# Kernel optimization log

Hardware: AMD Instinct MI355X
Metric: run time of the kernel (lower is better)

## Reference

```python
import jax, jax.numpy as jnp
import numpy as np

B, M, D, P, T = 512, 16, 128, 16, 4096
GAMMA = 1.0  # similarity_size


def setup_inputs() -> dict:
    key = jax.random.key(0)
    k1, k2, k3, k4, k5 = jax.random.split(key, 5)
    phi = jax.random.normal(k1, (B, P), dtype=jnp.float32)
    state = jax.random.normal(k2, (B, D), dtype=jnp.float32)
    trajectories = jax.random.normal(k3, (T, D), dtype=jnp.float32)
    # Stand-in per-model KAARMA state-transition parameters (linear recurrent + input map, tanh)
    A = jax.random.normal(k4, (M, D, D), dtype=jnp.float32) * (1.0 / np.sqrt(D))
    B_in = jax.random.normal(k5, (M, P, D), dtype=jnp.float32) * (1.0 / np.sqrt(P))
    return {"phi": phi, "state": state, "trajectories": trajectories, "A": A, "B_in": B_in}


def reference(phi, state, trajectories, A, B_in):
    # per-model state update: new_state[b,m,:] = tanh(state @ A_m + phi @ B_m)
    new_state = jnp.tanh(
        jnp.einsum("bd,mdh->bmh", state, A) + jnp.einsum("bp,mph->bmh", phi, B_in)
    )  # [B, M, D]
    # RBF similarity vs trajectory set via ||s||^2 + ||t||^2 - 2 s.t (single batched GEMM)
    s_sq = jnp.sum(new_state * new_state, axis=-1, keepdims=True)      # [B, M, 1]
    t_sq = jnp.sum(trajectories * trajectories, axis=-1)               # [T]
    cross = jnp.einsum("bmd,td->bmt", new_state, trajectories)         # [B, M, T]
    sq_dist = jnp.maximum(s_sq + t_sq[None, None, :] - 2.0 * cross, 0.0)
    sim = jnp.exp(-GAMMA * sq_dist)                                    # [B, M, T]
    output = sim.reshape(phi.shape[0], -1)                             # [B, M*T]
    return output, new_state
```

## Files before the change

kernel.cpp:

```cpp
#include <hip/hip_runtime.h>
#include <hip/hip_bf16.h>
#include <cstdint>
#include <cstddef>

#define NB 512
#define NM 16
#define ND 128
#define NP 16
#define NT 4096

typedef __bf16 bf16x8 __attribute__((ext_vector_type(8)));
typedef float f32x4 __attribute__((ext_vector_type(4)));

static_assert(sizeof(bf16x8) == 16, "bf16x8 must be 16B");

__device__ __forceinline__ void gload_lds16(const void* g, void* l) {
  __builtin_amdgcn_global_load_lds(
      (const __attribute__((address_space(1))) unsigned int*)g,
      (__attribute__((address_space(3))) unsigned int*)l, 16, 0, 0);
}

__global__ __launch_bounds__(256) void prep_kernel(
    const float* __restrict__ phi, const float* __restrict__ state,
    const float* __restrict__ traj, const float* __restrict__ A,
    const float* __restrict__ Bin, float* __restrict__ ns_out,
    __bf16* __restrict__ ns_bf, __bf16* __restrict__ tj_bf,
    float* __restrict__ s_sq, float* __restrict__ t_sq) {
  __shared__ alignas(16) float sSt[16 * 128];
  __shared__ alignas(16) float sPhi[16 * 16];
  __shared__ alignas(16) float sRes[16 * 128];
  const int tid = threadIdx.x;
  const int bx = blockIdx.x;

  if (bx < 512) {
    const int m = bx & 15;
    const int b0 = (bx >> 4) * 16;
    const float4* S4 = (const float4*)(state + (size_t)b0 * 128);
    float4* sSt4 = (float4*)sSt;
    sSt4[tid] = S4[tid];
    sSt4[tid + 256] = S4[tid + 256];
    sPhi[tid] = phi[b0 * 16 + tid];
    __syncthreads();

    const int h2 = tid & 63;
    const int rgrp = tid >> 6;
    const float* Ap = A + (size_t)m * 16384 + h2;
    const float* Bp = Bin + (size_t)m * 2048 + h2;

    float acc[2][4];
#pragma unroll
    for (int hi = 0; hi < 2; ++hi)
#pragma unroll
      for (int j = 0; j < 4; ++j) acc[hi][j] = 0.f;

#pragma unroll 4
    for (int c = 0; c < 32; ++c) {
      float a0[4], a1[4];
#pragma unroll
      for (int u = 0; u < 4; ++u) {
        a0[u] = Ap[(size_t)(c * 4 + u) * 128];
        a1[u] = Ap[(size_t)(c * 4 + u) * 128 + 64];
      }
#pragma unroll
      for (int j = 0; j < 4; ++j) {
        const f32x4 sv = *(const f32x4*)&sSt[(rgrp * 4 + j) * 128 + c * 4];
#pragma unroll
        for (int u = 0; u < 4; ++u) {
          acc[0][j] = fmaf(sv[u], a0[u], acc[0][j]);
          acc[1][j] = fmaf(sv[u], a1[u], acc[1][j]);
        }
      }
    }
#pragma unroll
    for (int pc = 0; pc < 4; ++pc) {
      float b0v[4], b1v[4];
#pragma unroll
      for (int u = 0; u < 4; ++u) {
        b0v[u] = Bp[(size_t)(pc * 4 + u) * 128];
        b1v[u] = Bp[(size_t)(pc * 4 + u) * 128 + 64];
      }
#pragma unroll
      for (int j = 0; j < 4; ++j) {
        const f32x4 pv = *(const f32x4*)&sPhi[(rgrp * 4 + j) * 16 + pc * 4];
#pragma unroll
        for (int u = 0; u < 4; ++u) {
          acc[0][j] = fmaf(pv[u], b0v[u], acc[0][j]);
          acc[1][j] = fmaf(pv[u], b1v[u], acc[1][j]);
        }
      }
    }

#pragma unroll
    for (int j = 0; j < 4; ++j) {
      const int row = rgrp * 4 + j;
      const int R = (b0 + row) * 16 + m;
      const float v0 = tanhf(acc[0][j]);
      const float v1 = tanhf(acc[1][j]);
      ns_out[(size_t)R * 128 + h2] = v0;
      ns_out[(size_t)R * 128 + h2 + 64] = v1;
      sRes[row * 128 + h2] = v0;
      sRes[row * 128 + h2 + 64] = v1;
      float s = v0 * v0 + v1 * v1;
#pragma unroll
      for (int o = 32; o > 0; o >>= 1) s += __shfl_xor(s, o);
      if (h2 == 0) s_sq[R] = s;
    }
    __syncthreads();

    {
      const int row = tid >> 4;
      const int kb = tid & 15;
      const f32x4 r0 = *(const f32x4*)&sRes[row * 128 + kb * 8];
      const f32x4 r1 = *(const f32x4*)&sRes[row * 128 + kb * 8 + 4];
      bf16x8 o;
#pragma unroll
      for (int i = 0; i < 4; ++i) {
        o[i] = (__bf16)r0[i];
        o[i + 4] = (__bf16)r1[i];
      }
      const int R = (b0 + row) * 16 + m;
      *(bf16x8*)(ns_bf + (size_t)R * 128 + ((kb ^ m) * 8)) = o;
    }
  } else {
    const int t0 = (bx - 512) * 128;
    const int t = t0 + (tid >> 1);
    const int half = tid & 1;
    float s = 0.f;
#pragma unroll
    for (int q = 0; q < 8; ++q) {
      const int kb = half * 8 + q;
      const f32x4 v0 = *(const f32x4*)&traj[(size_t)t * 128 + kb * 8];
      const f32x4 v1 = *(const f32x4*)&traj[(size_t)t * 128 + kb * 8 + 4];
      s += v0[0] * v0[0] + v0[1] * v0[1] + v0[2] * v0[2] + v0[3] * v0[3];
      s += v1[0] * v1[0] + v1[1] * v1[1] + v1[2] * v1[2] + v1[3] * v1[3];
      bf16x8 o;
#pragma unroll
      for (int i = 0; i < 4; ++i) {
        o[i] = (__bf16)v0[i];
        o[i + 4] = (__bf16)v1[i];
      }
      *(bf16x8*)(tj_bf + (size_t)t * 128 + ((kb ^ (t & 15)) * 8)) = o;
    }
    s += __shfl_xor(s, 1);
    if (half == 0) t_sq[t] = s;
  }
}

__global__ __launch_bounds__(256) void sim_kernel(
    const __bf16* __restrict__ ns_bf, const __bf16* __restrict__ tj_bf,
    const float* __restrict__ s_sq, const float* __restrict__ t_sq,
    float* __restrict__ out) {
  __shared__ alignas(16) __bf16 sA[128 * 128];
  __shared__ alignas(16) __bf16 sB[128 * 128];
  __shared__ float sSq[128];
  __shared__ float sTq[128];
  const int tid = threadIdx.x;
  const int lane = tid & 63;
  const int w = tid >> 6;
  const int R0 = blockIdx.x * 128;
  const int C0 = blockIdx.y * 128;

  const char* gA = (const char*)(ns_bf + (size_t)R0 * 128);
  const char* gB = (const char*)(tj_bf + (size_t)C0 * 128);
#pragma unroll
  for (int it = 0; it < 8; ++it) {
    const int off = it * 4096 + w * 1024;
    gload_lds16(gA + off + lane * 16, (char*)sA + off);
    gload_lds16(gB + off + lane * 16, (char*)sB + off);
  }
  if (tid < 128)
    sSq[tid] = s_sq[R0 + tid];
  else
    sTq[tid - 128] = t_sq[C0 + tid - 128];
  __syncthreads();

  const int rbase = (w >> 1) * 64;
  const int cbase = (w & 1) * 64;
  const int l15 = lane & 15;
  const int quad = lane >> 4;

  f32x4 acc[4][4];
#pragma unroll
  for (int i = 0; i < 4; ++i)
#pragma unroll
    for (int j = 0; j < 4; ++j) acc[i][j] = (f32x4){0.f, 0.f, 0.f, 0.f};

#pragma unroll
  for (int ks = 0; ks < 4; ++ks) {
    const int kb = quad + ks * 4;
    const int koff = (kb ^ l15) * 8;
    bf16x8 af[4], bfr[4];
#pragma unroll
    for (int i = 0; i < 4; ++i)
      af[i] = *(const bf16x8*)&sA[(rbase + i * 16 + l15) * 128 + koff];
#pragma unroll
    for (int i = 0; i < 4; ++i)
      bfr[i] = *(const bf16x8*)&sB[(cbase + i * 16 + l15) * 128 + koff];
#pragma unroll
    for (int ri = 0; ri < 4; ++ri)
#pragma unroll
      for (int ci = 0; ci < 4; ++ci)
        acc[ri][ci] = __builtin_amdgcn_mfma_f32_16x16x32_bf16(
            bfr[ci], af[ri], acc[ri][ci], 0, 0, 0);
  }

#pragma unroll
  for (int ri = 0; ri < 4; ++ri) {
    const int nsrow = rbase + ri * 16 + l15;
    const float sq = sSq[nsrow];
    float* orow = out + (size_t)(R0 + nsrow) * NT + C0;
#pragma unroll
    for (int ci = 0; ci < 4; ++ci) {
      const int t4 = cbase + ci * 16 + quad * 4;
      const f32x4 tq = *(const f32x4*)&sTq[t4];
      f32x4 r;
#pragma unroll
      for (int k = 0; k < 4; ++k) {
        const float d = fmaxf(sq + tq[k] - 2.f * acc[ri][ci][k], 0.f);
        r[k] = __expf(-d);
      }
      *(f32x4*)&orow[t4] = r;
    }
  }
}

extern "C" void kernel_launch(void* const* d_in, const int* in_sizes, int n_in,
                              void* d_out, int out_size, void* d_ws,
                              size_t ws_size, hipStream_t stream) {
  (void)in_sizes; (void)n_in; (void)out_size; (void)ws_size;
  const float* phi   = (const float*)d_in[0];
  const float* state = (const float*)d_in[1];
  const float* traj  = (const float*)d_in[2];
  const float* A     = (const float*)d_in[3];
  const float* Bin   = (const float*)d_in[4];

  float* out = (float*)d_out;
  float* out_ns = out + (size_t)NB * NM * NT;

  char* ws = (char*)d_ws;
  __bf16* ns_bf = (__bf16*)ws;
  __bf16* tj_bf = (__bf16*)(ws + (2u << 20));
  float* s_sq   = (float*)(ws + (3u << 20));
  float* t_sq   = (float*)(ws + (3u << 20) + (32u << 10));

  prep_kernel<<<544, 256, 0, stream>>>(phi, state, traj, A, Bin, out_ns, ns_bf,
                                       tj_bf, s_sq, t_sq);
  dim3 g2(NB * NM / 128, NT / 128);
  sim_kernel<<<g2, 256, 0, stream>>>(ns_bf, tj_bf, s_sq, t_sq, out);
}
```

Before: 168.7 us.

## Halve sim-kernel A tile in LDS, process rows in two halves, nontemporal stores

The sim kernel now keeps only 64 rows of the state tile in LDS and handles the 128-row block in two halves. The second half is loaded while the first half's epilogue runs. This cuts LDS use (48KB instead of 64KB) and accumulator registers, so more blocks can be resident per CU and output stores can overlap with loads. All output and new_state stores become nontemporal so they do not pollute the cache. The cost is extra barriers and a serialized second GEMM phase per block.

```diff
diff --git a/kernel.cpp b/kernel.cpp
--- a/kernel.cpp
+++ b/kernel.cpp
@@ -96,8 +96,8 @@
       const int R = (b0 + row) * 16 + m;
       const float v0 = tanhf(acc[0][j]);
       const float v1 = tanhf(acc[1][j]);
-      ns_out[(size_t)R * 128 + h2] = v0;
-      ns_out[(size_t)R * 128 + h2 + 64] = v1;
+      __builtin_nontemporal_store(v0, &ns_out[(size_t)R * 128 + h2]);
+      __builtin_nontemporal_store(v1, &ns_out[(size_t)R * 128 + h2 + 64]);
       sRes[row * 128 + h2] = v0;
       sRes[row * 128 + h2 + 64] = v1;
       float s = v0 * v0 + v1 * v1;
@@ -150,8 +150,8 @@
     const __bf16* __restrict__ ns_bf, const __bf16* __restrict__ tj_bf,
     const float* __restrict__ s_sq, const float* __restrict__ t_sq,
     float* __restrict__ out) {
-  __shared__ alignas(16) __bf16 sA[128 * 128];
   __shared__ alignas(16) __bf16 sB[128 * 128];
+  __shared__ alignas(16) __bf16 sA[64 * 128];
   __shared__ float sSq[128];
   __shared__ float sTq[128];
   const int tid = threadIdx.x;
@@ -160,13 +160,17 @@
   const int R0 = blockIdx.x * 128;
   const int C0 = blockIdx.y * 128;
 
+  const char* gB = (const char*)(tj_bf + (size_t)C0 * 128);
   const char* gA = (const char*)(ns_bf + (size_t)R0 * 128);
-  const char* gB = (const char*)(tj_bf + (size_t)C0 * 128);
 #pragma unroll
   for (int it = 0; it < 8; ++it) {
-    const int off = it * 4096 + w * 1024;
+    const int off = w * 8192 + it * 1024;
+    gload_lds16(gB + off + lane * 16, (char*)sB + off);
+  }
+#pragma unroll
+  for (int it = 0; it < 4; ++it) {
+    const int off = w * 4096 + it * 1024;
     gload_lds16(gA + off + lane * 16, (char*)sA + off);
-    gload_lds16(gB + off + lane * 16, (char*)sB + off);
   }
   if (tid < 128)
     sSq[tid] = s_sq[R0 + tid];
@@ -174,53 +178,68 @@
     sTq[tid - 128] = t_sq[C0 + tid - 128];
   __syncthreads();
 
-  const int rbase = (w >> 1) * 64;
+  const int abase = (w >> 1) * 32;
   const int cbase = (w & 1) * 64;
   const int l15 = lane & 15;
   const int quad = lane >> 4;
 
-  f32x4 acc[4][4];
-#pragma unroll
-  for (int i = 0; i < 4; ++i)
-#pragma unroll
-    for (int j = 0; j < 4; ++j) acc[i][j] = (f32x4){0.f, 0.f, 0.f, 0.f};
-
-#pragma unroll
-  for (int ks = 0; ks < 4; ++ks) {
-    const int kb = quad + ks * 4;
-    const int koff = (kb ^ l15) * 8;
-    bf16x8 af[4], bfr[4];
-#pragma unroll
-    for (int i = 0; i < 4; ++i)
-      af[i] = *(const bf16x8*)&sA[(rbase + i * 16 + l15) * 128 + koff];
-#pragma unroll
-    for (int i = 0; i < 4; ++i)
-      bfr[i] = *(const bf16x8*)&sB[(cbase + i * 16 + l15) * 128 + koff];
-#pragma unroll
-    for (int ri = 0; ri < 4; ++ri)
-#pragma unroll
-      for (int ci = 0; ci < 4; ++ci)
-        acc[ri][ci] = __builtin_amdgcn_mfma_f32_16x16x32_bf16(
-            bfr[ci], af[ri], acc[ri][ci], 0, 0, 0);
-  }
-
-#pragma unroll
-  for (int ri = 0; ri < 4; ++ri) {
-    const int nsrow = rbase + ri * 16 + l15;
-    const float sq = sSq[nsrow];
-    float* orow = out + (size_t)(R0 + nsrow) * NT + C0;
-#pragma unroll
-    for (int ci = 0; ci < 4; ++ci) {
-      const int t4 = cbase + ci * 16 + quad * 4;
-      const f32x4 tq = *(const f32x4*)&sTq[t4];
-      f32x4 r;
-#pragma unroll
-      for (int k = 0; k < 4; ++k) {
-        const float d = fmaxf(sq + tq[k] - 2.f * acc[ri][ci][k], 0.f);
-        r[k] = __expf(-d);
-      }
-      *(f32x4*)&orow[t4] = r;
-    }
+  f32x4 acc[2][4];
+
+#pragma unroll
+  for (int half = 0; half < 2; ++half) {
+#pragma unroll
+    for (int i = 0; i < 2; ++i)
+#pragma unroll
+      for (int j = 0; j < 4; ++j) acc[i][j] = (f32x4){0.f, 0.f, 0.f, 0.f};
+
+#pragma unroll
+    for (int ks = 0; ks < 4; ++ks) {
+      const int kb = quad + ks * 4;
+      const int koff = (kb ^ l15) * 8;
+      bf16x8 af[2], bfr[4];
+#pragma unroll
+      for (int i = 0; i < 2; ++i)
+        af[i] = *(const bf16x8*)&sA[(abase + i * 16 + l15) * 128 + koff];
+#pragma unroll
+      for (int i = 0; i < 4; ++i)
+        bfr[i] = *(const bf16x8*)&sB[(cbase + i * 16 + l15) * 128 + koff];
+#pragma unroll
+      for (int ri = 0; ri < 2; ++ri)
+#pragma unroll
+        for (int ci = 0; ci < 4; ++ci)
+          acc[ri][ci] = __builtin_amdgcn_mfma_f32_16x16x32_bf16(
+              bfr[ci], af[ri], acc[ri][ci], 0, 0, 0);
+    }
+
+    if (half == 0) {
+      __syncthreads();
+#pragma unroll
+      for (int it = 0; it < 4; ++it) {
+        const int off = w * 4096 + it * 1024;
+        gload_lds16(gA + 16384 + off + lane * 16, (char*)sA + off);
+      }
+    }
+
+#pragma unroll
+    for (int ri = 0; ri < 2; ++ri) {
+      const int lrow = half * 64 + abase + ri * 16 + l15;
+      const float sq = sSq[lrow];
+      float* orow = out + (size_t)(R0 + lrow) * NT + C0;
+#pragma unroll
+      for (int ci = 0; ci < 4; ++ci) {
+        const int t4 = cbase + ci * 16 + quad * 4;
+        const f32x4 tq = *(const f32x4*)&sTq[t4];
+        f32x4 r;
+#pragma unroll
+        for (int k = 0; k < 4; ++k) {
+          const float d = fmaxf(sq + tq[k] - 2.f * acc[ri][ci][k], 0.f);
+          r[k] = __expf(-d);
+        }
+        __builtin_nontemporal_store(r, (f32x4*)&orow[t4]);
+      }
+    }
+
+    if (half == 0) __syncthreads();
   }
 }
 
```

New measurement: 214.8 us. +27.3%, slower.
